# Performance work log

Hardware: AMD Instinct MI355X
Metric: run time of the kernel (lower is better)

Reference implementation:

```python
import jax, jax.numpy as jnp
import numpy as np

N = 50000
NUM_FEATURES = 128
HIDDEN = 64
NUM_CLASSES = 32
K_HOPS = 4
E = 1600000
CST = 1e-05


def setup_inputs() -> dict:
    key = jax.random.key(0)
    ks = jax.random.split(key, 12)
    def lin(k, fan_in, fan_out):
        b = 1.0 / np.sqrt(fan_in)
        kw, kb = jax.random.split(k)
        W = jax.random.uniform(kw, (fan_in, fan_out), jnp.float32, -b, b)
        bias = jax.random.uniform(kb, (fan_out,), jnp.float32, -b, b)
        return W, bias
    W_in, b_in = lin(ks[0], NUM_FEATURES, HIDDEN)
    WQ, bQ = lin(ks[1], HIDDEN, HIDDEN)
    WK, bK = lin(ks[2], HIDDEN, HIDDEN)
    WV, bV = lin(ks[3], HIDDEN, NUM_CLASSES)
    return {
        'node_feat': jax.random.normal(ks[4], (N, NUM_FEATURES), jnp.float32),
        'W_in': W_in, 'b_in': b_in,
        'WQ': WQ, 'bQ': bQ,
        'WK': WK, 'bK': bK,
        'WV': WV, 'bV': bV,
        'hopwise': jnp.ones((K_HOPS + 1,), jnp.float32),
        'teleport': jnp.ones((1,), jnp.float32),
        'edge_index': jax.random.randint(ks[5], (2, E), 0, N, jnp.int64 if jax.config.jax_enable_x64 else jnp.int32),
    }


def reference(node_feat, W_in, b_in, WQ, bQ, WK, bK, WV, bV, hopwise, teleport, edge_index):
    n = node_feat.shape[0]
    row, col = edge_index[0], edge_index[1]
    # random-walk norm: deg over targets (col), inverted, indexed at sources (row)
    deg = jax.ops.segment_sum(jnp.ones_like(row, node_feat.dtype), col, num_segments=n)
    deg_inv = jnp.where(deg > 0, 1.0 / deg, 0.0)
    norm = deg_inv[row]  # [E]

    x = jax.nn.relu(node_feat @ W_in + b_in)          # [n, h]
    Q = 1.0 + jax.nn.elu(x @ WQ + bQ)                 # [n, h]
    Kf = 1.0 + jax.nn.elu(x @ WK + bK)                # [n, h]
    V = x @ WV + bV                                   # [n, c]
    M = jnp.einsum('ni,nj->nij', Kf, V)               # [n, h, c]

    # global attention (teleport) branch
    teleportM = jnp.sum(M, axis=0) / n                # [h, c]
    teleportK = jnp.sum(Kf, axis=0) / n               # [h]
    teleportH = jnp.einsum('ni,ij->nj', Q, teleportM)
    teleportC = jnp.einsum('ni,i->n', Q, teleportK)[:, None] + CST
    teleportH = teleportH / teleportC

    hidden = V * hopwise[0]
    for hop in range(K_HOPS):
        # edge gather -> weight -> scatter-sum (message passing)
        M = jax.ops.segment_sum(norm[:, None, None] * M[row], col, num_segments=n)
        Kf = jax.ops.segment_sum(norm[:, None] * Kf[row], col, num_segments=n)
        H = jnp.einsum('ni,nij->nj', Q, M)
        C = jnp.sum(Q * Kf, axis=-1, keepdims=True) + CST
        hidden = hidden + hopwise[hop + 1] * (H / C)

    hidden = hidden + teleport * teleportH
    return hidden
```

## Files before the change

kernel.cpp:

```cpp
#include <hip/hip_runtime.h>
#include <math.h>
#include <stdint.h>

#define NN 50000
#define FIN 128
#define HD 64
#define CD 32
#define EE 1600000
#define CSTV 1e-5f
#define NB 49

typedef unsigned short u16;
typedef unsigned int u32;
typedef unsigned char u8;
typedef unsigned int uv2 __attribute__((ext_vector_type(2)));
typedef unsigned int uv4 __attribute__((ext_vector_type(4)));
typedef float fv2 __attribute__((ext_vector_type(2)));

static __device__ __forceinline__ float b2f(u16 u){
  union { float f; u32 i; } v; v.i = ((u32)u) << 16; return v.f;
}
static __device__ __forceinline__ u16 f2b(float f){
  union { float f; u32 u; } v; v.f = f;
  u32 u = v.u;
  u32 r = (u + 0x7fffu + ((u >> 16) & 1u)) >> 16;
  return (u16)r;
}
static __device__ __forceinline__ float ldin(const void* p, size_t i, int isf){
  return isf ? ((const float*)p)[i] : b2f(((const u16*)p)[i]);
}

static __device__ __forceinline__ void dec8(u32 g, float* f){
  fv2 lo = __builtin_amdgcn_cvt_pk_f32_fp8(g, false);
  fv2 hi = __builtin_amdgcn_cvt_pk_f32_fp8(g, true);
  f[0] = lo.x; f[1] = lo.y; f[2] = hi.x; f[3] = hi.y;
}
static __device__ __forceinline__ u32 enc8(const float* f){
  u32 r = 0;
  r = __builtin_amdgcn_cvt_pk_fp8_f32(f[0], f[1], r, false);
  r = __builtin_amdgcn_cvt_pk_fp8_f32(f[2], f[3], r, true);
  return r;
}
template<int C>
static __device__ __forceinline__ void loadF8(const u8* __restrict__ p, float* f){
  if constexpr (C == 32){
    uint4 g0 = ((const uint4*)p)[0];
    uint4 g1 = ((const uint4*)p)[1];
    dec8(g0.x, f+0);  dec8(g0.y, f+4);  dec8(g0.z, f+8);  dec8(g0.w, f+12);
    dec8(g1.x, f+16); dec8(g1.y, f+20); dec8(g1.z, f+24); dec8(g1.w, f+28);
  } else if constexpr (C == 16){
    uint4 g = *(const uint4*)p;
    dec8(g.x, f+0); dec8(g.y, f+4); dec8(g.z, f+8); dec8(g.w, f+12);
  } else {
    uint2 g = *(const uint2*)p;
    dec8(g.x, f+0); dec8(g.y, f+4);
  }
}
template<int C>
static __device__ __forceinline__ void storeF8NT(u8* __restrict__ p, const float* f){
  if constexpr (C == 32){
    uv4 g0, g1;
    g0.x=enc8(f+0);  g0.y=enc8(f+4);  g0.z=enc8(f+8);  g0.w=enc8(f+12);
    g1.x=enc8(f+16); g1.y=enc8(f+20); g1.z=enc8(f+24); g1.w=enc8(f+28);
    __builtin_nontemporal_store(g0, (uv4*)p);
    __builtin_nontemporal_store(g1, (uv4*)p + 1);
  } else if constexpr (C == 16){
    uv4 g; g.x=enc8(f+0); g.y=enc8(f+4); g.z=enc8(f+8); g.w=enc8(f+12);
    __builtin_nontemporal_store(g, (uv4*)p);
  } else {
    uv2 g; g.x=enc8(f+0); g.y=enc8(f+4);
    __builtin_nontemporal_store(g, (uv2*)p);
  }
}
template<int C>
static __device__ __forceinline__ void loadB(const u16* __restrict__ p, float* f){
  if constexpr (C == 32){
    #pragma unroll
    for (int q = 0; q < 4; ++q){
      uint4 g = ((const uint4*)p)[q];
      f[q*8+0]=b2f((u16)(g.x&0xffff)); f[q*8+1]=b2f((u16)(g.x>>16));
      f[q*8+2]=b2f((u16)(g.y&0xffff)); f[q*8+3]=b2f((u16)(g.y>>16));
      f[q*8+4]=b2f((u16)(g.z&0xffff)); f[q*8+5]=b2f((u16)(g.z>>16));
      f[q*8+6]=b2f((u16)(g.w&0xffff)); f[q*8+7]=b2f((u16)(g.w>>16));
    }
  } else if constexpr (C == 16){
    #pragma unroll
    for (int q = 0; q < 2; ++q){
      uint4 g = ((const uint4*)p)[q];
      f[q*8+0]=b2f((u16)(g.x&0xffff)); f[q*8+1]=b2f((u16)(g.x>>16));
      f[q*8+2]=b2f((u16)(g.y&0xffff)); f[q*8+3]=b2f((u16)(g.y>>16));
      f[q*8+4]=b2f((u16)(g.z&0xffff)); f[q*8+5]=b2f((u16)(g.z>>16));
      f[q*8+6]=b2f((u16)(g.w&0xffff)); f[q*8+7]=b2f((u16)(g.w>>16));
    }
  } else {
    uint4 g = *(const uint4*)p;
    f[0]=b2f((u16)(g.x&0xffff)); f[1]=b2f((u16)(g.x>>16));
    f[2]=b2f((u16)(g.y&0xffff)); f[3]=b2f((u16)(g.y>>16));
    f[4]=b2f((u16)(g.z&0xffff)); f[5]=b2f((u16)(g.z>>16));
    f[6]=b2f((u16)(g.w&0xffff)); f[7]=b2f((u16)(g.w>>16));
  }
}

__global__ void k_detect(const u16* __restrict__ w, int* __restrict__ flag){
  __shared__ int bad;
  if (threadIdx.x == 0) bad = 0;
  __syncthreads();
  for (int i = threadIdx.x; i < 2048; i += 256){
    float v = b2f(w[i]);
    if (!(fabsf(v) <= 1.0f)) bad = 1;
  }
  __syncthreads();
  if (threadIdx.x == 0) flag[0] = bad;
}


__global__ void k_zero(int* cnt, float* teleM, float* teleK){
  int i = blockIdx.x * 256 + threadIdx.x;
  if (i < NN) cnt[i] = 0;
  if (i < HD * CD) teleM[i] = 0.f;
  if (i < HD) teleK[i] = 0.f;
}

__global__ void k_hist(const int* __restrict__ colp, int* __restrict__ cnt){
  int e = blockIdx.x * 256 + threadIdx.x;
  if (e < EE) atomicAdd(&cnt[colp[e]], 1);
}

__global__ __launch_bounds__(1024) void k_scanA(const int* __restrict__ cnt,
                                                int* __restrict__ loc, int* __restrict__ bsum){
  __shared__ int wsum[16];
  int t = threadIdx.x; int i = blockIdx.x * 1024 + t;
  int v = (i < NN) ? cnt[i] : 0;
  int x = v;
  int lane = t & 63, wid = t >> 6;
  #pragma unroll
  for (int d = 1; d < 64; d <<= 1){ int n = __shfl_up(x, d, 64); if (lane >= d) x += n; }
  if (lane == 63) wsum[wid] = x;
  __syncthreads();
  if (t < 16){
    int y = wsum[t];
    #pragma unroll
    for (int d = 1; d < 16; d <<= 1){ int n = __shfl_up(y, d, 16); if (t >= d) y += n; }
    wsum[t] = y;
  }
  __syncthreads();
  if (wid > 0) x += wsum[wid - 1];
  if (i < NN) loc[i] = x;
  if (t == 1023) bsum[blockIdx.x] = x;
}

__global__ __launch_bounds__(64) void k_scanB(const int* __restrict__ bsum,
                                              int* __restrict__ boff, int* __restrict__ ptrNN){
  int t = threadIdx.x;
  int v = (t < NB) ? bsum[t] : 0;
  int x = v;
  #pragma unroll
  for (int d = 1; d < 64; d <<= 1){ int n = __shfl_up(x, d, 64); if (t >= d) x += n; }
  if (t < NB) boff[t] = x - v;
  if (t == 63) ptrNN[0] = x;
}

__global__ __launch_bounds__(1024) void k_scanC(const int* __restrict__ cnt, const int* __restrict__ loc,
                                                const int* __restrict__ boff, int* __restrict__ ptr,
                                                int* __restrict__ fill, float* __restrict__ dinv){
  int i = blockIdx.x * 1024 + threadIdx.x;
  if (i < NN){
    int c = cnt[i];
    int p = boff[blockIdx.x] + loc[i] - c;
    ptr[i] = p; fill[i] = p;
    dinv[i] = (c > 0) ? 1.f / (float)c : 0.f;
  }
}

__global__ void k_scatter(const int* __restrict__ rowp, const int* __restrict__ colp,
                          const float* __restrict__ dinv, int* __restrict__ fill,
                          int2* __restrict__ ew){
  int e = blockIdx.x * 256 + threadIdx.x;
  if (e < EE){
    int c = colp[e];
    int p = atomicAdd(&fill[c], 1);
    int r = rowp[e];
    int2 v; v.x = r; v.y = __float_as_int(dinv[r]);
    ew[p] = v;
  }
}


__global__ __launch_bounds__(256) void k_x(const void* __restrict__ feat, const void* __restrict__ Win,
                                           const void* __restrict__ bin, const int* __restrict__ fl,
                                           float* __restrict__ x){
  int isf = fl[0];
  __shared__ float Ws[FIN * HD];
  __shared__ float fs[4 * FIN];
  __shared__ float bs[HD];
  int t = threadIdx.x;
  for (int idx = t; idx < FIN * HD; idx += 256) Ws[idx] = ldin(Win, idx, isf);
  if (t < HD) bs[t] = ldin(bin, t, isf);
  int n0 = blockIdx.x * 4;
  for (int idx = t; idx < 4 * FIN; idx += 256){
    int nl = idx >> 7, k = idx & 127; int n = n0 + nl;
    fs[idx] = (n < NN) ? ldin(feat, (size_t)n * FIN + k, isf) : 0.f;
  }
  __syncthreads();
  int nl = t >> 6, o = t & 63; int n = n0 + nl;
  if (n < NN){
    float acc = bs[o];
    #pragma unroll 8
    for (int k = 0; k < FIN; ++k) acc += fs[nl * FIN + k] * Ws[k * HD + o];
    x[(size_t)n * HD + o] = fmaxf(acc, 0.f);
  }
}

__global__ __launch_bounds__(256) void k_qkv(const float* __restrict__ x,
    const void* __restrict__ WQ, const void* __restrict__ bQ,
    const void* __restrict__ WK, const void* __restrict__ bK,
    const void* __restrict__ WV, const void* __restrict__ bV,
    const void* __restrict__ hopwise, const int* __restrict__ fl,
    float* __restrict__ Q, u16* __restrict__ Kf0b, u16* __restrict__ Vb,
    float* __restrict__ hid){
  int isf = fl[0];
  __shared__ float WQs[HD * HD], WKs[HD * HD], WVs[HD * CD];
  __shared__ float bqs[HD], bks[HD], bvs[CD];
  __shared__ float xs[4 * HD];
  int t = threadIdx.x;
  for (int idx = t; idx < HD * HD; idx += 256){ WQs[idx] = ldin(WQ, idx, isf); WKs[idx] = ldin(WK, idx, isf); }
  for (int idx = t; idx < HD * CD; idx += 256) WVs[idx] = ldin(WV, idx, isf);
  if (t < HD){ bqs[t] = ldin(bQ, t, isf); bks[t] = ldin(bK, t, isf); }
  if (t < CD) bvs[t] = ldin(bV, t, isf);
  int n0 = blockIdx.x * 4;
  for (int idx = t; idx < 4 * HD; idx += 256){
    int nl = idx >> 6; int n = n0 + nl;
    xs[idx] = (n < NN) ? x[(size_t)n * HD + (idx & 63)] : 0.f;
  }
  __syncthreads();
  int nl = t >> 6, o = t & 63; int n = n0 + nl;
  float hw0 = ldin(hopwise, 0, isf);
  float q = bqs[o], kf = bks[o];
  #pragma unroll 8
  for (int k = 0; k < HD; ++k){
    float xv = xs[nl * HD + k];
    q  += xv * WQs[k * HD + o];
    kf += xv * WKs[k * HD + o];
  }
  q  = (q  > 0.f) ? 1.f + q  : expf(q);
  kf = (kf > 0.f) ? 1.f + kf : expf(kf);
  if (n < NN){ Q[(size_t)n * HD + o] = q; Kf0b[(size_t)n * HD + o] = f2b(kf); }
  if (o < CD && n < NN){
    float v = bvs[o];
    #pragma unroll 8
    for (int k = 0; k < HD; ++k) v += xs[nl * HD + k] * WVs[k * CD + o];
    Vb[(size_t)n * CD + o] = f2b(v);
    hid[(size_t)n * CD + o] = hw0 * v;
  }
}


__global__ __launch_bounds__(256) void k_tele(const u16* __restrict__ Kf0b, const u16* __restrict__ Vb,
                                              float* __restrict__ teleM, float* __restrict__ teleK){
  __shared__ float accM[HD * CD];
  __shared__ float accKs[HD];
  __shared__ float KfL[HD];
  __shared__ float VL[CD];
  int t = threadIdx.x;
  for (int idx = t; idx < HD * CD; idx += 256) accM[idx] = 0.f;
  if (t < HD) accKs[t] = 0.f;
  __syncthreads();
  for (int n = blockIdx.x; n < NN; n += gridDim.x){
    if (t < HD) KfL[t] = b2f(Kf0b[(size_t)n * HD + t]);
    else if (t < HD + CD) VL[t - HD] = b2f(Vb[(size_t)n * CD + (t - HD)]);
    __syncthreads();
    for (int idx = t; idx < HD * CD; idx += 256){
      int h = idx >> 5, c = idx & 31;
      accM[idx] += KfL[h] * VL[c];
    }
    if (t < HD) accKs[t] += KfL[t];
    __syncthreads();
  }
  for (int idx = t; idx < HD * CD; idx += 256) atomicAdd(&teleM[idx], accM[idx]);
  if (t < HD) atomicAdd(&teleK[t], accKs[t]);
}


template<int C, bool FIRST, bool FUSEK, bool LAST>
__global__ __launch_bounds__(128)
void k_hop(const u8* __restrict__ Min, const u16* __restrict__ Kf0b, const u16* __restrict__ Vb,
           const u16* __restrict__ KfIn, u16* __restrict__ KfOut,
           const float* __restrict__ Qb, const int2* __restrict__ ew, const int* __restrict__ ptr,
           float* __restrict__ invC, const void* __restrict__ hopw, const int* __restrict__ fl,
           int hopidx, u8* __restrict__ Mout, float* __restrict__ hid, int c0){
  int wv = threadIdx.x >> 6;
  int t = threadIdx.x & 63;
  int i = blockIdx.x * 2 + wv;
  int e0 = __builtin_amdgcn_readfirstlane(ptr[i]);
  int e1 = __builtin_amdgcn_readfirstlane(ptr[i + 1]);
  float a[C];
  #pragma unroll
  for (int j = 0; j < C; ++j) a[j] = 0.f;
  float accK = 0.f;
  int e = e0;
  if constexpr (FIRST){
    for (; e + 2 <= e1; e += 2){
      int2 d0 = ew[e], d1 = ew[e+1];
      float s0 = __int_as_float(d0.y) * b2f(Kf0b[(size_t)d0.x * HD + t]);
      float s1 = __int_as_float(d1.y) * b2f(Kf0b[(size_t)d1.x * HD + t]);
      float v0[C], v1[C];
      loadB<C>(Vb + (size_t)d0.x * CD + c0, v0);
      loadB<C>(Vb + (size_t)d1.x * CD + c0, v1);
      #pragma unroll
      for (int j = 0; j < C; ++j) a[j] += s0 * v0[j] + s1 * v1[j];
      if constexpr (FUSEK) accK += s0 + s1;
    }
    for (; e < e1; ++e){
      int2 d0 = ew[e];
      float s0 = __int_as_float(d0.y) * b2f(Kf0b[(size_t)d0.x * HD + t]);
      float v0[C];
      loadB<C>(Vb + (size_t)d0.x * CD + c0, v0);
      #pragma unroll
      for (int j = 0; j < C; ++j) a[j] += s0 * v0[j];
      if constexpr (FUSEK) accK += s0;
    }
  } else {
    for (; e + 2 <= e1; e += 2){
      int2 d0 = ew[e], d1 = ew[e+1];
      float w0 = __int_as_float(d0.y), w1 = __int_as_float(d1.y);
      float m0[C], m1[C];
      loadF8<C>(Min + (size_t)d0.x * (HD * C) + t * C, m0);
      loadF8<C>(Min + (size_t)d1.x * (HD * C) + t * C, m1);
      if constexpr (FUSEK){
        accK += w0 * b2f(KfIn[(size_t)d0.x * HD + t]) + w1 * b2f(KfIn[(size_t)d1.x * HD + t]);
      }
      #pragma unroll
      for (int j = 0; j < C; ++j) a[j] += w0 * m0[j] + w1 * m1[j];
    }
    for (; e < e1; ++e){
      int2 d0 = ew[e];
      float w0 = __int_as_float(d0.y);
      float m0[C];
      loadF8<C>(Min + (size_t)d0.x * (HD * C) + t * C, m0);
      if constexpr (FUSEK) accK += w0 * b2f(KfIn[(size_t)d0.x * HD + t]);
      #pragma unroll
      for (int j = 0; j < C; ++j) a[j] += w0 * m0[j];
    }
  }
  float q = Qb[(size_t)i * HD + t];
  float ic;
  if constexpr (FUSEK){
    if constexpr (!LAST) KfOut[(size_t)i * HD + t] = f2b(accK);
    float ck = q * accK;
    #pragma unroll
    for (int off = 32; off >= 1; off >>= 1) ck += __shfl_down(ck, off, 64);
    ck = 1.f / (ck + CSTV);
    if (t == 0) invC[i] = ck;
    ic = ck;
  } else {
    ic = invC[i];
  }
  float p[C];
  #pragma unroll
  for (int j = 0; j < C; ++j) p[j] = q * a[j];
  #pragma unroll
  for (int off = 32; off >= 1; off >>= 1){
    #pragma unroll
    for (int j = 0; j < C; ++j) p[j] += __shfl_down(p[j], off, 64);
  }
  if (t == 0){
    float coef = ldin(hopw, hopidx, fl[0]) * ic;
    float* hp = hid + (size_t)i * CD + c0;
    #pragma unroll
    for (int j = 0; j < C; ++j) hp[j] += coef * p[j];
  }
  if constexpr (!LAST) storeF8NT<C>(Mout + (size_t)i * (HD * C) + t * C, a);
}


__global__ __launch_bounds__(256) void k_final(const float* __restrict__ hid, const float* __restrict__ Qb,
    const float* __restrict__ teleM, const float* __restrict__ teleK, const void* __restrict__ tel,
    const int* __restrict__ fl, void* __restrict__ out){
  int isf = fl[0];
  __shared__ float tM[HD * CD];
  __shared__ float tK[HD];
  int t = threadIdx.x;
  for (int idx = t; idx < HD * CD; idx += 256) tM[idx] = teleM[idx];
  if (t < HD) tK[t] = teleK[t];
  __syncthreads();
  int nl = t >> 5, c = t & 31;
  int n = blockIdx.x * 8 + nl;
  if (n < NN){
    const float* q = Qb + (size_t)n * HD;
    float dH = 0.f, dK = 0.f;
    #pragma unroll 8
    for (int h = 0; h < HD; ++h){
      float qv = q[h];
      dH += qv * tM[h * CD + c];
      dK += qv * tK[h];
    }
    float invn = 1.f / (float)NN;
    float tH = (dH * invn) / (dK * invn + CSTV);
    float val = hid[(size_t)n * CD + c] + ldin(tel, 0, isf) * tH;
    if (isf) ((float*)out)[(size_t)n * CD + c] = val;
    else ((u16*)out)[(size_t)n * CD + c] = f2b(val);
  }
}


template<int C>
static void launch_chunks(u8* Ma, u8* Mb, const u16* Kf0b, const u16* Vb,
                          u16* KfPa, u16* KfPb, const float* Q, const int2* ew,
                          const int* ptr, float* invC, const void* hop, const int* flag,
                          float* hid, hipStream_t stream){
  int nchunks = CD / C;
  int grid = NN / 2;
  for (int ch = 0; ch < nchunks; ++ch){
    int c0 = ch * C;
    if (ch == 0){
      k_hop<C,true ,true ,false><<<grid,128,0,stream>>>(nullptr, Kf0b, Vb, nullptr, KfPa, Q, ew, ptr, invC+0*NN, hop, flag, 1, Ma, hid, c0);
      k_hop<C,false,true ,false><<<grid,128,0,stream>>>(Ma, Kf0b, Vb, KfPa, KfPb, Q, ew, ptr, invC+1*NN, hop, flag, 2, Mb, hid, c0);
      k_hop<C,false,true ,false><<<grid,128,0,stream>>>(Mb, Kf0b, Vb, KfPb, KfPa, Q, ew, ptr, invC+2*NN, hop, flag, 3, Ma, hid, c0);
      k_hop<C,false,true ,true ><<<grid,128,0,stream>>>(Ma, Kf0b, Vb, KfPa, nullptr, Q, ew, ptr, invC+3*NN, hop, flag, 4, nullptr, hid, c0);
    } else {
      k_hop<C,true ,false,false><<<grid,128,0,stream>>>(nullptr, Kf0b, Vb, nullptr, nullptr, Q, ew, ptr, invC+0*NN, hop, flag, 1, Ma, hid, c0);
      k_hop<C,false,false,false><<<grid,128,0,stream>>>(Ma, Kf0b, Vb, nullptr, nullptr, Q, ew, ptr, invC+1*NN, hop, flag, 2, Mb, hid, c0);
      k_hop<C,false,false,false><<<grid,128,0,stream>>>(Mb, Kf0b, Vb, nullptr, nullptr, Q, ew, ptr, invC+2*NN, hop, flag, 3, Ma, hid, c0);
      k_hop<C,false,false,true ><<<grid,128,0,stream>>>(Ma, Kf0b, Vb, nullptr, nullptr, Q, ew, ptr, invC+3*NN, hop, flag, 4, nullptr, hid, c0);
    }
  }
}


extern "C" void kernel_launch(void* const* d_in, const int* in_sizes, int n_in,
                              void* d_out, int out_size, void* d_ws, size_t ws_size,
                              hipStream_t stream){
  const void* feat = d_in[0];
  const void* Win  = d_in[1];
  const void* bin  = d_in[2];
  const void* WQ   = d_in[3];
  const void* bQ   = d_in[4];
  const void* WK   = d_in[5];
  const void* bK   = d_in[6];
  const void* WV   = d_in[7];
  const void* bV   = d_in[8];
  const void* hop  = d_in[9];
  const void* tel  = d_in[10];
  const int* ei    = (const int*)d_in[11];
  const int* rowp  = ei;
  const int* colp  = ei + EE;

  char* w = (char*)d_ws;
  size_t off = 0;
  auto pad = [](size_t x){ return (x + 255) & ~((size_t)255); };
  auto alloc = [&](size_t bytes) -> char* {
    char* p = w + off;
    off += pad(bytes);
    return p;
  };
  float* Q    = (float*)alloc((size_t)NN * HD * 4);
  float* hid  = (float*)alloc((size_t)NN * CD * 4);
  float* invC = (float*)alloc((size_t)4 * NN * 4);
  float* dinv = (float*)alloc((size_t)NN * 4);
  int*   cnt  = (int*)alloc((size_t)NN * 4);
  int*   ptr  = (int*)alloc((size_t)(NN + 1) * 4);
  int*   fill = (int*)alloc((size_t)NN * 4);
  int*   bsum = (int*)alloc(64 * 4);
  int*   boff = (int*)alloc(64 * 4);
  int2*  ew   = (int2*)alloc((size_t)EE * 8);
  float* teleM= (float*)alloc((size_t)HD * CD * 4);
  float* teleK= (float*)alloc((size_t)HD * 4);
  int*   flag = (int*)alloc(256);
  u16*   Kf0b = (u16*)alloc((size_t)NN * HD * 2);
  u16*   KfPa = (u16*)alloc((size_t)NN * HD * 2);
  u16*   KfPb = (u16*)alloc((size_t)NN * HD * 2);
  u16*   Vb   = (u16*)alloc((size_t)NN * CD * 2);

  size_t fixed = off;
  auto fits = [&](int C){ return fixed + 2 * pad((size_t)NN * HD * C) <= ws_size; };
  int C = fits(32) ? 32 : (fits(16) ? 16 : 8);
  size_t mbytes = pad((size_t)NN * HD * C);
  char* mreg = alloc(2 * mbytes);
  u8* Ma = (u8*)mreg;
  u8* Mb = (u8*)(mreg + mbytes);
  float* x = (float*)mreg;

  k_detect<<<1, 256, 0, stream>>>((const u16*)Win, flag);
  k_zero<<<(NN + 255) / 256, 256, 0, stream>>>(cnt, teleM, teleK);
  k_hist<<<(EE + 255) / 256, 256, 0, stream>>>(colp, cnt);
  k_scanA<<<NB, 1024, 0, stream>>>(cnt, fill, bsum);
  k_scanB<<<1, 64, 0, stream>>>(bsum, boff, ptr + NN);
  k_scanC<<<NB, 1024, 0, stream>>>(cnt, fill, boff, ptr, fill, dinv);
  k_scatter<<<(EE + 255) / 256, 256, 0, stream>>>(rowp, colp, dinv, fill, ew);
  k_x<<<(NN + 3) / 4, 256, 0, stream>>>(feat, Win, bin, flag, x);
  k_qkv<<<(NN + 3) / 4, 256, 0, stream>>>(x, WQ, bQ, WK, bK, WV, bV, hop, flag, Q, Kf0b, Vb, hid);
  k_tele<<<256, 256, 0, stream>>>(Kf0b, Vb, teleM, teleK);

  if (C == 32)      launch_chunks<32>(Ma, Mb, Kf0b, Vb, KfPa, KfPb, Q, ew, ptr, invC, hop, flag, hid, stream);
  else if (C == 16) launch_chunks<16>(Ma, Mb, Kf0b, Vb, KfPa, KfPb, Q, ew, ptr, invC, hop, flag, hid, stream);
  else              launch_chunks<8 >(Ma, Mb, Kf0b, Vb, KfPa, KfPb, Q, ew, ptr, invC, hop, flag, hid, stream);

  k_final<<<(NN + 7) / 8, 256, 0, stream>>>(hid, Q, teleM, teleK, tel, flag, d_out);
}
```

Before: 2.279 ms.

## Fuse feature and QKV projections, store V in fp32, scalarize edge indices

Merges the input projection and QKV projection into one kernel that keeps x in shared memory, with bf16 weights in LDS and 8 nodes per block. It also folds the detect kernel into the zero kernel and raises the teleport-reduction grid to 1024 blocks. V is now stored in fp32, and the first hop makes edge indices wave-uniform with readfirstlane so the V loads can go through scalar or broadcast paths. The aim is fewer launches and less x round-trip traffic, at the cost of a larger V buffer and bf16 rounding of the weights.

```diff
diff --git a/kernel.cpp b/kernel.cpp
--- a/kernel.cpp
+++ b/kernel.cpp
@@ -72,54 +72,26 @@
     __builtin_nontemporal_store(g, (uv2*)p);
   }
 }
-template<int C>
-static __device__ __forceinline__ void loadB(const u16* __restrict__ p, float* f){
-  if constexpr (C == 32){
-    #pragma unroll
-    for (int q = 0; q < 4; ++q){
-      uint4 g = ((const uint4*)p)[q];
-      f[q*8+0]=b2f((u16)(g.x&0xffff)); f[q*8+1]=b2f((u16)(g.x>>16));
-      f[q*8+2]=b2f((u16)(g.y&0xffff)); f[q*8+3]=b2f((u16)(g.y>>16));
-      f[q*8+4]=b2f((u16)(g.z&0xffff)); f[q*8+5]=b2f((u16)(g.z>>16));
-      f[q*8+6]=b2f((u16)(g.w&0xffff)); f[q*8+7]=b2f((u16)(g.w>>16));
-    }
-  } else if constexpr (C == 16){
-    #pragma unroll
-    for (int q = 0; q < 2; ++q){
-      uint4 g = ((const uint4*)p)[q];
-      f[q*8+0]=b2f((u16)(g.x&0xffff)); f[q*8+1]=b2f((u16)(g.x>>16));
-      f[q*8+2]=b2f((u16)(g.y&0xffff)); f[q*8+3]=b2f((u16)(g.y>>16));
-      f[q*8+4]=b2f((u16)(g.z&0xffff)); f[q*8+5]=b2f((u16)(g.z>>16));
-      f[q*8+6]=b2f((u16)(g.w&0xffff)); f[q*8+7]=b2f((u16)(g.w>>16));
-    }
-  } else {
-    uint4 g = *(const uint4*)p;
-    f[0]=b2f((u16)(g.x&0xffff)); f[1]=b2f((u16)(g.x>>16));
-    f[2]=b2f((u16)(g.y&0xffff)); f[3]=b2f((u16)(g.y>>16));
-    f[4]=b2f((u16)(g.z&0xffff)); f[5]=b2f((u16)(g.z>>16));
-    f[6]=b2f((u16)(g.w&0xffff)); f[7]=b2f((u16)(g.w>>16));
-  }
-}
-
-__global__ void k_detect(const u16* __restrict__ w, int* __restrict__ flag){
-  __shared__ int bad;
-  if (threadIdx.x == 0) bad = 0;
-  __syncthreads();
-  for (int i = threadIdx.x; i < 2048; i += 256){
-    float v = b2f(w[i]);
-    if (!(fabsf(v) <= 1.0f)) bad = 1;
-  }
-  __syncthreads();
-  if (threadIdx.x == 0) flag[0] = bad;
-}
-
-
-__global__ void k_zero(int* cnt, float* teleM, float* teleK){
+
+__global__ void k_zero(const u16* __restrict__ w, int* __restrict__ flag,
+                       int* cnt, float* teleM, float* teleK){
   int i = blockIdx.x * 256 + threadIdx.x;
   if (i < NN) cnt[i] = 0;
   if (i < HD * CD) teleM[i] = 0.f;
   if (i < HD) teleK[i] = 0.f;
-}
+  if (blockIdx.x == 0){
+    __shared__ int bad;
+    if (threadIdx.x == 0) bad = 0;
+    __syncthreads();
+    for (int k = threadIdx.x; k < 2048; k += 256){
+      float v = b2f(w[k]);
+      if (!(fabsf(v) <= 1.0f)) bad = 1;
+    }
+    __syncthreads();
+    if (threadIdx.x == 0) flag[0] = bad;
+  }
+}
+
 
 __global__ void k_hist(const int* __restrict__ colp, int* __restrict__ cnt){
   int e = blockIdx.x * 256 + threadIdx.x;
@@ -186,76 +158,74 @@
 }
 
 
-__global__ __launch_bounds__(256) void k_x(const void* __restrict__ feat, const void* __restrict__ Win,
-                                           const void* __restrict__ bin, const int* __restrict__ fl,
-                                           float* __restrict__ x){
-  int isf = fl[0];
-  __shared__ float Ws[FIN * HD];
-  __shared__ float fs[4 * FIN];
-  __shared__ float bs[HD];
-  int t = threadIdx.x;
-  for (int idx = t; idx < FIN * HD; idx += 256) Ws[idx] = ldin(Win, idx, isf);
-  if (t < HD) bs[t] = ldin(bin, t, isf);
-  int n0 = blockIdx.x * 4;
-  for (int idx = t; idx < 4 * FIN; idx += 256){
-    int nl = idx >> 7, k = idx & 127; int n = n0 + nl;
-    fs[idx] = (n < NN) ? ldin(feat, (size_t)n * FIN + k, isf) : 0.f;
-  }
-  __syncthreads();
-  int nl = t >> 6, o = t & 63; int n = n0 + nl;
-  if (n < NN){
-    float acc = bs[o];
-    #pragma unroll 8
-    for (int k = 0; k < FIN; ++k) acc += fs[nl * FIN + k] * Ws[k * HD + o];
-    x[(size_t)n * HD + o] = fmaxf(acc, 0.f);
-  }
-}
-
-__global__ __launch_bounds__(256) void k_qkv(const float* __restrict__ x,
+__global__ __launch_bounds__(256) void k_feat(
+    const void* __restrict__ feat, const void* __restrict__ Win, const void* __restrict__ bin,
     const void* __restrict__ WQ, const void* __restrict__ bQ,
     const void* __restrict__ WK, const void* __restrict__ bK,
     const void* __restrict__ WV, const void* __restrict__ bV,
     const void* __restrict__ hopwise, const int* __restrict__ fl,
-    float* __restrict__ Q, u16* __restrict__ Kf0b, u16* __restrict__ Vb,
+    float* __restrict__ Q, u16* __restrict__ Kf0b, float* __restrict__ V32,
     float* __restrict__ hid){
   int isf = fl[0];
-  __shared__ float WQs[HD * HD], WKs[HD * HD], WVs[HD * CD];
-  __shared__ float bqs[HD], bks[HD], bvs[CD];
-  __shared__ float xs[4 * HD];
+  __shared__ u16 Ws[FIN * HD];
+  __shared__ u16 WQs[HD * HD];
+  __shared__ u16 WKs[HD * HD];
+  __shared__ u16 WVs[HD * CD];
+  __shared__ float bs[HD], bqs[HD], bks[HD], bvs[CD];
+  __shared__ float fs[8 * FIN];
+  __shared__ float xs[8 * HD];
   int t = threadIdx.x;
-  for (int idx = t; idx < HD * HD; idx += 256){ WQs[idx] = ldin(WQ, idx, isf); WKs[idx] = ldin(WK, idx, isf); }
-  for (int idx = t; idx < HD * CD; idx += 256) WVs[idx] = ldin(WV, idx, isf);
-  if (t < HD){ bqs[t] = ldin(bQ, t, isf); bks[t] = ldin(bK, t, isf); }
+  for (int idx = t; idx < FIN * HD; idx += 256) Ws[idx] = f2b(ldin(Win, idx, isf));
+  for (int idx = t; idx < HD * HD; idx += 256){
+    WQs[idx] = f2b(ldin(WQ, idx, isf));
+    WKs[idx] = f2b(ldin(WK, idx, isf));
+  }
+  for (int idx = t; idx < HD * CD; idx += 256) WVs[idx] = f2b(ldin(WV, idx, isf));
+  if (t < HD){ bs[t] = ldin(bin, t, isf); bqs[t] = ldin(bQ, t, isf); bks[t] = ldin(bK, t, isf); }
   if (t < CD) bvs[t] = ldin(bV, t, isf);
-  int n0 = blockIdx.x * 4;
-  for (int idx = t; idx < 4 * HD; idx += 256){
-    int nl = idx >> 6; int n = n0 + nl;
-    xs[idx] = (n < NN) ? x[(size_t)n * HD + (idx & 63)] : 0.f;
-  }
-  __syncthreads();
-  int nl = t >> 6, o = t & 63; int n = n0 + nl;
+  int n0 = blockIdx.x * 8;
+  for (int idx = t; idx < 8 * FIN; idx += 256){
+    int nl = idx >> 7, k = idx & 127; int n = n0 + nl;
+    fs[idx] = (n < NN) ? ldin(feat, (size_t)n * FIN + k, isf) : 0.f;
+  }
+  __syncthreads();
+  int o = t & 63, g = t >> 6;
+  #pragma unroll
+  for (int rep = 0; rep < 2; ++rep){
+    int nl = g + rep * 4;
+    float acc = bs[o];
+    #pragma unroll 8
+    for (int k = 0; k < FIN; ++k) acc += fs[nl * FIN + k] * b2f(Ws[k * HD + o]);
+    xs[nl * HD + o] = fmaxf(acc, 0.f);
+  }
+  __syncthreads();
   float hw0 = ldin(hopwise, 0, isf);
-  float q = bqs[o], kf = bks[o];
-  #pragma unroll 8
-  for (int k = 0; k < HD; ++k){
-    float xv = xs[nl * HD + k];
-    q  += xv * WQs[k * HD + o];
-    kf += xv * WKs[k * HD + o];
-  }
-  q  = (q  > 0.f) ? 1.f + q  : expf(q);
-  kf = (kf > 0.f) ? 1.f + kf : expf(kf);
-  if (n < NN){ Q[(size_t)n * HD + o] = q; Kf0b[(size_t)n * HD + o] = f2b(kf); }
-  if (o < CD && n < NN){
-    float v = bvs[o];
+  #pragma unroll
+  for (int rep = 0; rep < 2; ++rep){
+    int nl = g + rep * 4; int n = n0 + nl;
+    float q = bqs[o], kf = bks[o];
     #pragma unroll 8
-    for (int k = 0; k < HD; ++k) v += xs[nl * HD + k] * WVs[k * CD + o];
-    Vb[(size_t)n * CD + o] = f2b(v);
-    hid[(size_t)n * CD + o] = hw0 * v;
-  }
-}
-
-
-__global__ __launch_bounds__(256) void k_tele(const u16* __restrict__ Kf0b, const u16* __restrict__ Vb,
+    for (int k = 0; k < HD; ++k){
+      float xv = xs[nl * HD + k];
+      q  += xv * b2f(WQs[k * HD + o]);
+      kf += xv * b2f(WKs[k * HD + o]);
+    }
+    q  = (q  > 0.f) ? 1.f + q  : expf(q);
+    kf = (kf > 0.f) ? 1.f + kf : expf(kf);
+    if (n < NN){ Q[(size_t)n * HD + o] = q; Kf0b[(size_t)n * HD + o] = f2b(kf); }
+  }
+  int nv = t >> 5, c = t & 31; int n = n0 + nv;
+  if (n < NN){
+    float v = bvs[c];
+    #pragma unroll 8
+    for (int k = 0; k < HD; ++k) v += xs[nv * HD + k] * b2f(WVs[k * CD + c]);
+    V32[(size_t)n * CD + c] = v;
+    hid[(size_t)n * CD + c] = hw0 * v;
+  }
+}
+
+
+__global__ __launch_bounds__(256) void k_tele(const u16* __restrict__ Kf0b, const float* __restrict__ V32,
                                               float* __restrict__ teleM, float* __restrict__ teleK){
   __shared__ float accM[HD * CD];
   __shared__ float accKs[HD];
@@ -267,7 +237,7 @@
   __syncthreads();
   for (int n = blockIdx.x; n < NN; n += gridDim.x){
     if (t < HD) KfL[t] = b2f(Kf0b[(size_t)n * HD + t]);
-    else if (t < HD + CD) VL[t - HD] = b2f(Vb[(size_t)n * CD + (t - HD)]);
+    else if (t < HD + CD) VL[t - HD] = V32[(size_t)n * CD + (t - HD)];
     __syncthreads();
     for (int idx = t; idx < HD * CD; idx += 256){
       int h = idx >> 5, c = idx & 31;
@@ -283,7 +253,7 @@
 
 template<int C, bool FIRST, bool FUSEK, bool LAST>
 __global__ __launch_bounds__(128)
-void k_hop(const u8* __restrict__ Min, const u16* __restrict__ Kf0b, const u16* __restrict__ Vb,
+void k_hop(const u8* __restrict__ Min, const u16* __restrict__ Kf0b, const float* __restrict__ V32,
            const u16* __restrict__ KfIn, u16* __restrict__ KfOut,
            const float* __restrict__ Qb, const int2* __restrict__ ew, const int* __restrict__ ptr,
            float* __restrict__ invC, const void* __restrict__ hopw, const int* __restrict__ fl,
@@ -301,22 +271,26 @@
   if constexpr (FIRST){
     for (; e + 2 <= e1; e += 2){
       int2 d0 = ew[e], d1 = ew[e+1];
-      float s0 = __int_as_float(d0.y) * b2f(Kf0b[(size_t)d0.x * HD + t]);
-      float s1 = __int_as_float(d1.y) * b2f(Kf0b[(size_t)d1.x * HD + t]);
-      float v0[C], v1[C];
-      loadB<C>(Vb + (size_t)d0.x * CD + c0, v0);
-      loadB<C>(Vb + (size_t)d1.x * CD + c0, v1);
+      int r0 = __builtin_amdgcn_readfirstlane(d0.x);
+      int r1 = __builtin_amdgcn_readfirstlane(d1.x);
+      float w0 = __int_as_float(__builtin_amdgcn_readfirstlane(d0.y));
+      float w1 = __int_as_float(__builtin_amdgcn_readfirstlane(d1.y));
+      float s0 = w0 * b2f(Kf0b[(size_t)r0 * HD + t]);
+      float s1 = w1 * b2f(Kf0b[(size_t)r1 * HD + t]);
+      const float* vp0 = V32 + (size_t)r0 * CD + c0;
+      const float* vp1 = V32 + (size_t)r1 * CD + c0;
       #pragma unroll
-      for (int j = 0; j < C; ++j) a[j] += s0 * v0[j] + s1 * v1[j];
+      for (int j = 0; j < C; ++j) a[j] += s0 * vp0[j] + s1 * vp1[j];
       if constexpr (FUSEK) accK += s0 + s1;
     }
     for (; e < e1; ++e){
       int2 d0 = ew[e];
-      float s0 = __int_as_float(d0.y) * b2f(Kf0b[(size_t)d0.x * HD + t]);
-      float v0[C];
-      loadB<C>(Vb + (size_t)d0.x * CD + c0, v0);
+      int r0 = __builtin_amdgcn_readfirstlane(d0.x);
+      float w0 = __int_as_float(__builtin_amdgcn_readfirstlane(d0.y));
+      float s0 = w0 * b2f(Kf0b[(size_t)r0 * HD + t]);
+      const float* vp0 = V32 + (size_t)r0 * CD + c0;
       #pragma unroll
-      for (int j = 0; j < C; ++j) a[j] += s0 * v0[j];
+      for (int j = 0; j < C; ++j) a[j] += s0 * vp0[j];
       if constexpr (FUSEK) accK += s0;
     }
   } else {
@@ -404,7 +378,7 @@
 
 
 template<int C>
-static void launch_chunks(u8* Ma, u8* Mb, const u16* Kf0b, const u16* Vb,
+static void launch_chunks(u8* Ma, u8* Mb, const u16* Kf0b, const float* V32,
                           u16* KfPa, u16* KfPb, const float* Q, const int2* ew,
                           const int* ptr, float* invC, const void* hop, const int* flag,
                           float* hid, hipStream_t stream){
@@ -413,15 +387,15 @@
   for (int ch = 0; ch < nchunks; ++ch){
     int c0 = ch * C;
     if (ch == 0){
-      k_hop<C,true ,true ,false><<<grid,128,0,stream>>>(nullptr, Kf0b, Vb, nullptr, KfPa, Q, ew, ptr, invC+0*NN, hop, flag, 1, Ma, hid, c0);
-      k_hop<C,false,true ,false><<<grid,128,0,stream>>>(Ma, Kf0b, Vb, KfPa, KfPb, Q, ew, ptr, invC+1*NN, hop, flag, 2, Mb, hid, c0);
-      k_hop<C,false,true ,false><<<grid,128,0,stream>>>(Mb, Kf0b, Vb, KfPb, KfPa, Q, ew, ptr, invC+2*NN, hop, flag, 3, Ma, hid, c0);
-      k_hop<C,false,true ,true ><<<grid,128,0,stream>>>(Ma, Kf0b, Vb, KfPa, nullptr, Q, ew, ptr, invC+3*NN, hop, flag, 4, nullptr, hid, c0);
+      k_hop<C,true ,true ,false><<<grid,128,0,stream>>>(nullptr, Kf0b, V32, nullptr, KfPa, Q, ew, ptr, invC+0*NN, hop, flag, 1, Ma, hid, c0);
+      k_hop<C,false,true ,false><<<grid,128,0,stream>>>(Ma, Kf0b, V32, KfPa, KfPb, Q, ew, ptr, invC+1*NN, hop, flag, 2, Mb, hid, c0);
+      k_hop<C,false,true ,false><<<grid,128,0,stream>>>(Mb, Kf0b, V32, KfPb, KfPa, Q, ew, ptr, invC+2*NN, hop, flag, 3, Ma, hid, c0);
+      k_hop<C,false,true ,true ><<<grid,128,0,stream>>>(Ma, Kf0b, V32, KfPa, nullptr, Q, ew, ptr, invC+3*NN, hop, flag, 4, nullptr, hid, c0);
     } else {
-      k_hop<C,true ,false,false><<<grid,128,0,stream>>>(nullptr, Kf0b, Vb, nullptr, nullptr, Q, ew, ptr, invC+0*NN, hop, flag, 1, Ma, hid, c0);
-      k_hop<C,false,false,false><<<grid,128,0,stream>>>(Ma, Kf0b, Vb, nullptr, nullptr, Q, ew, ptr, invC+1*NN, hop, flag, 2, Mb, hid, c0);
-      k_hop<C,false,false,false><<<grid,128,0,stream>>>(Mb, Kf0b, Vb, nullptr, nullptr, Q, ew, ptr, invC+2*NN, hop, flag, 3, Ma, hid, c0);
-      k_hop<C,false,false,true ><<<grid,128,0,stream>>>(Ma, Kf0b, Vb, nullptr, nullptr, Q, ew, ptr, invC+3*NN, hop, flag, 4, nullptr, hid, c0);
+      k_hop<C,true ,false,false><<<grid,128,0,stream>>>(nullptr, Kf0b, V32, nullptr, nullptr, Q, ew, ptr, invC+0*NN, hop, flag, 1, Ma, hid, c0);
+      k_hop<C,false,false,false><<<grid,128,0,stream>>>(Ma, Kf0b, V32, nullptr, nullptr, Q, ew, ptr, invC+1*NN, hop, flag, 2, Mb, hid, c0);
+      k_hop<C,false,false,false><<<grid,128,0,stream>>>(Mb, Kf0b, V32, nullptr, nullptr, Q, ew, ptr, invC+2*NN, hop, flag, 3, Ma, hid, c0);
+      k_hop<C,false,false,true ><<<grid,128,0,stream>>>(Ma, Kf0b, V32, nullptr, nullptr, Q, ew, ptr, invC+3*NN, hop, flag, 4, nullptr, hid, c0);
     }
   }
 }
@@ -469,7 +443,7 @@
   u16*   Kf0b = (u16*)alloc((size_t)NN * HD * 2);
   u16*   KfPa = (u16*)alloc((size_t)NN * HD * 2);
   u16*   KfPb = (u16*)alloc((size_t)NN * HD * 2);
-  u16*   Vb   = (u16*)alloc((size_t)NN * CD * 2);
+  float* V32  = (float*)alloc((size_t)NN * CD * 4);
 
   size_t fixed = off;
   auto fits = [&](int C){ return fixed + 2 * pad((size_t)NN * HD * C) <= ws_size; };
@@ -478,22 +452,20 @@
   char* mreg = alloc(2 * mbytes);
   u8* Ma = (u8*)mreg;
   u8* Mb = (u8*)(mreg + mbytes);
-  float* x = (float*)mreg;
-
-  k_detect<<<1, 256, 0, stream>>>((const u16*)Win, flag);
-  k_zero<<<(NN + 255) / 256, 256, 0, stream>>>(cnt, teleM, teleK);
+
+  k_zero<<<(NN + 255) / 256, 256, 0, stream>>>((const u16*)Win, flag, cnt, teleM, teleK);
   k_hist<<<(EE + 255) / 256, 256, 0, stream>>>(colp, cnt);
   k_scanA<<<NB, 1024, 0, stream>>>(cnt, fill, bsum);
   k_scanB<<<1, 64, 0, stream>>>(bsum, boff, ptr + NN);
   k_scanC<<<NB, 1024, 0, stream>>>(cnt, fill, boff, ptr, fill, dinv);
   k_scatter<<<(EE + 255) / 256, 256, 0, stream>>>(rowp, colp, dinv, fill, ew);
-  k_x<<<(NN + 3) / 4, 256, 0, stream>>>(feat, Win, bin, flag, x);
-  k_qkv<<<(NN + 3) / 4, 256, 0, stream>>>(x, WQ, bQ, WK, bK, WV, bV, hop, flag, Q, Kf0b, Vb, hid);
-  k_tele<<<256, 256, 0, stream>>>(Kf0b, Vb, teleM, teleK);
-
-  if (C == 32)      launch_chunks<32>(Ma, Mb, Kf0b, Vb, KfPa, KfPb, Q, ew, ptr, invC, hop, flag, hid, stream);
-  else if (C == 16) launch_chunks<16>(Ma, Mb, Kf0b, Vb, KfPa, KfPb, Q, ew, ptr, invC, hop, flag, hid, stream);
-  else              launch_chunks<8 >(Ma, Mb, Kf0b, Vb, KfPa, KfPb, Q, ew, ptr, invC, hop, flag, hid, stream);
+  k_feat<<<(NN + 7) / 8, 256, 0, stream>>>(feat, Win, bin, WQ, bQ, WK, bK, WV, bV,
+                                           hop, flag, Q, Kf0b, V32, hid);
+  k_tele<<<1024, 256, 0, stream>>>(Kf0b, V32, teleM, teleK);
+
+  if (C == 32)      launch_chunks<32>(Ma, Mb, Kf0b, V32, KfPa, KfPb, Q, ew, ptr, invC, hop, flag, hid, stream);
+  else if (C == 16) launch_chunks<16>(Ma, Mb, Kf0b, V32, KfPa, KfPb, Q, ew, ptr, invC, hop, flag, hid, stream);
+  else              launch_chunks<8 >(Ma, Mb, Kf0b, V32, KfPa, KfPb, Q, ew, ptr, invC, hop, flag, hid, stream);
 
   k_final<<<(NN + 7) / 8, 256, 0, stream>>>(hid, Q, teleM, teleK, tel, flag, d_out);
 }
```

After: 2.106 ms. -7.6%, faster.
